# Kernel optimization log

Hardware: AMD Instinct MI355X
Metric: run time of the kernel (lower is better)

## Reference

```python
import jax, jax.numpy as jnp
import numpy as np

B, S, D, H = 4, 1024, 1024, 16
HD = D // H


def setup_inputs() -> dict:
    key = jax.random.key(0)
    ks = jax.random.split(key, 12)
    s = 1.0 / np.sqrt(D)
    inp = {
        'q': jax.random.normal(ks[0], (B, S, D), jnp.float32),
        'k': jax.random.normal(ks[1], (B, S, D), jnp.float32),
        'v': jax.random.normal(ks[2], (B, S, D), jnp.float32),
        'mask': jnp.broadcast_to(jnp.tril(jnp.ones((S, S), jnp.int32)), (B, S, S)),
        'Wq': jax.random.uniform(ks[3], (D, D), jnp.float32, -s, s),
        'bq': jax.random.uniform(ks[4], (D,), jnp.float32, -s, s),
        'Wk': jax.random.uniform(ks[5], (D, D), jnp.float32, -s, s),
        'bk': jax.random.uniform(ks[6], (D,), jnp.float32, -s, s),
        'Wv': jax.random.uniform(ks[7], (D, D), jnp.float32, -s, s),
        'bv': jax.random.uniform(ks[8], (D,), jnp.float32, -s, s),
        'Wo': jax.random.uniform(ks[9], (D, D), jnp.float32, -s, s),
        'bo': jax.random.uniform(ks[10], (D,), jnp.float32, -s, s),
    }
    return inp


def _split_heads(x):
    # [B,S,D] -> [B,H,S,HD]
    b, s, d = x.shape
    return x.reshape(b, s, H, HD).transpose(0, 2, 1, 3)


def reference(q, k, v, mask, Wq, bq, Wk, bk, Wv, bv, Wo, bo):
    # Linear projections (torch Linear: x @ W.T + b) followed by relu
    qh = jax.nn.relu(q @ Wq.T + bq)
    kh = jax.nn.relu(k @ Wk.T + bk)
    vh = jax.nn.relu(v @ Wv.T + bv)
    qh, kh, vh = _split_heads(qh), _split_heads(kh), _split_heads(vh)
    scores = jnp.einsum('bhqd,bhkd->bhqk', qh, kh) / jnp.sqrt(jnp.float32(HD))
    scores = jnp.where(mask[:, None, :, :] == 0, jnp.float32(-1e9), scores)
    attn = jax.nn.softmax(scores, axis=-1)
    y = jnp.einsum('bhqk,bhkd->bhqd', attn, vh)
    y = y.transpose(0, 2, 1, 3).reshape(B, S, D)  # merge heads
    return jax.nn.relu(y @ Wo.T + bo)
```

## Files before the change

kernel.cpp:

```cpp
#include <hip/hip_runtime.h>


using f16    = _Float16;
using f16x4  = __attribute__((ext_vector_type(4))) _Float16;
using f16x8  = __attribute__((ext_vector_type(8))) _Float16;
using f32x4  = __attribute__((ext_vector_type(4))) float;
using f32x16 = __attribute__((ext_vector_type(16))) float;

static constexpr int S = 1024, Dm = 1024, NH = 16, HD = 64;

#if __has_builtin(__builtin_amdgcn_mfma_f32_32x32x8f16)
#define USE_MFMA32 1
#define MFMA32(ACC, A_, B_) \
    (ACC) = __builtin_amdgcn_mfma_f32_32x32x8f16((A_), (B_), (ACC), 0, 0, 0)
#else
#define USE_MFMA32 0
#endif
#if __has_builtin(__builtin_amdgcn_mfma_f32_16x16x16f16)
#define USE_MFMA 1
#define MFMA16(ACC, A_, B_) \
    (ACC) = __builtin_amdgcn_mfma_f32_16x16x16f16((A_), (B_), (ACC), 0, 0, 0)
#else
#define USE_MFMA 0
#endif

#define LO4(v) __builtin_shufflevector((v), (v), 0, 1, 2, 3)
#define HI4(v) __builtin_shufflevector((v), (v), 4, 5, 6, 7)

__device__ __forceinline__ f16x4 cvt4(float4 a) {
    f16x4 r; r[0] = (f16)a.x; r[1] = (f16)a.y; r[2] = (f16)a.z; r[3] = (f16)a.w;
    return r;
}
__device__ __forceinline__ int pcol64(int k) {
    return ((k >> 2) & 3) * 16 + ((k >> 4) << 2) + (k & 3);
}

__device__ __forceinline__ void store_out(void* out, int mode, int m, int n, float v) {
    if (mode == 2) {
        ((float*)out)[(size_t)m * Dm + n] = v;
    } else {
        const int b_ = m >> 10, s_ = m & 1023, h_ = n >> 6, hd_ = n & 63;
        const size_t idx = (mode == 0)
            ? (((size_t)(b_ * NH + h_) * S + s_) * HD + pcol64(hd_))
            : (((size_t)(b_ * NH + h_) * HD + hd_) * S + s_);
        ((f16*)out)[idx] = (f16)v;
    }
}

template <int AF32>
__device__ __forceinline__ void gemm_core(const void* __restrict__ A,
                                          const float* __restrict__ W,
                                          const float* __restrict__ bias,
                                          void* __restrict__ out, int mode)
{
    const int tid = threadIdx.x;
    const int bm = blockIdx.x, bn = blockIdx.y;
#if USE_MFMA32
    __shared__ alignas(16) f16 As[2][128][36];
    __shared__ alignas(16) f16 Ws[2][128][36];

    const int lane = tid & 63, wave = tid >> 6;
    const int l31 = lane & 31, kh = lane >> 5;
    const int wm = wave & 1, wn = wave >> 1;

    const int ar = tid >> 3, ac = (tid & 7) * 4;
    const int ar2 = tid >> 2, ac2 = (tid & 3) * 8;
    const float* Af = (const float*)A + (size_t)(bm * 128 + ar) * Dm + ac;
    const f16*   Ah = (const f16*)A   + (size_t)(bm * 128 + ar2) * Dm + ac2;
    const float* Wf = W + (size_t)(bn * 128 + ar) * Dm + ac;

    float4 pa[4]; uint4 pah[2]; float4 pw[4];
    auto pref = [&](int k0) {
        if (AF32) {
#pragma unroll
            for (int i = 0; i < 4; ++i) pa[i] = *(const float4*)(Af + k0 + (size_t)i * 32 * Dm);
        } else {
#pragma unroll
            for (int i = 0; i < 2; ++i) pah[i] = *(const uint4*)(Ah + k0 + (size_t)i * 64 * Dm);
        }
#pragma unroll
        for (int i = 0; i < 4; ++i) pw[i] = *(const float4*)(Wf + k0 + (size_t)i * 32 * Dm);
    };
    auto stage = [&](int cur) {
        if (AF32) {
#pragma unroll
            for (int i = 0; i < 4; ++i) *(f16x4*)&As[cur][ar + i * 32][ac] = cvt4(pa[i]);
        } else {
#pragma unroll
            for (int i = 0; i < 2; ++i) *(f16x8*)&As[cur][ar2 + i * 64][ac2] = *(f16x8*)&pah[i];
        }
#pragma unroll
        for (int i = 0; i < 4; ++i) *(f16x4*)&Ws[cur][ar + i * 32][ac] = cvt4(pw[i]);
    };

    f32x16 acc[2][2] = {};
    pref(0);
    for (int it = 0; it < Dm / 32; ++it) {
        const int cur = it & 1;
        stage(cur);
        __syncthreads();
        if (it < Dm / 32 - 1) pref((it + 1) * 32);

#pragma unroll
        for (int s = 0; s < 4; ++s) {
            f16x4 af[2], bf[2];
            const int c = s * 8 + kh * 4;
            af[0] = *(const f16x4*)&As[cur][wm * 64 + l31][c];
            af[1] = *(const f16x4*)&As[cur][wm * 64 + 32 + l31][c];
            bf[0] = *(const f16x4*)&Ws[cur][wn * 64 + l31][c];
            bf[1] = *(const f16x4*)&Ws[cur][wn * 64 + 32 + l31][c];
            MFMA32(acc[0][0], af[0], bf[0]);
            MFMA32(acc[0][1], af[0], bf[1]);
            MFMA32(acc[1][0], af[1], bf[0]);
            MFMA32(acc[1][1], af[1], bf[1]);
        }
    }

#pragma unroll
    for (int g2 = 0; g2 < 2; ++g2) {
        const int col = bn * 128 + wn * 64 + g2 * 32 + l31;
        const float bb = bias[col];
#pragma unroll
        for (int g = 0; g < 2; ++g)
#pragma unroll
            for (int blk = 0; blk < 4; ++blk) {
                const int row0 = bm * 128 + wm * 64 + g * 32 + 8 * blk + 4 * kh;
                if (mode == 1) {
                    const int b_ = row0 >> 10, s_ = row0 & 1023;
                    const int h_ = col >> 6, hd_ = col & 63;
                    f16x4 v;
#pragma unroll
                    for (int r = 0; r < 4; ++r)
                        v[r] = (f16)fmaxf(acc[g][g2][blk * 4 + r] + bb, 0.0f);
                    *(f16x4*)&((f16*)out)[((size_t)(b_ * NH + h_) * HD + hd_) * S + s_] = v;
                } else {
#pragma unroll
                    for (int r = 0; r < 4; ++r)
                        store_out(out, mode, row0 + r, col,
                                  fmaxf(acc[g][g2][blk * 4 + r] + bb, 0.0f));
                }
            }
    }
#else
    for (int i = tid; i < 128 * 128; i += 256) {
        const int m = bm * 128 + (i >> 7);
        const int n = bn * 128 + (i & 127);
        float acc = 0.0f;
        for (int k = 0; k < Dm; ++k) {
            const float a = AF32 ? ((const float*)A)[(size_t)m * Dm + k]
                                 : (float)((const f16*)A)[(size_t)m * Dm + k];
            acc = fmaf(a, W[(size_t)n * Dm + k], acc);
        }
        store_out(out, mode, m, n, fmaxf(acc + bias[n], 0.0f));
    }
#endif
}

__global__ __launch_bounds__(256)
void gemm_qkv(const float* __restrict__ q, const float* __restrict__ k,
              const float* __restrict__ v,
              const float* __restrict__ Wq, const float* __restrict__ Wk,
              const float* __restrict__ Wv,
              const float* __restrict__ bq, const float* __restrict__ bk,
              const float* __restrict__ bv,
              f16* __restrict__ qh, f16* __restrict__ kh, f16* __restrict__ vt)
{
    const int z = blockIdx.z;
    const float* A = (z == 0) ? q : (z == 1) ? k : v;
    const float* W = (z == 0) ? Wq : (z == 1) ? Wk : Wv;
    const float* B = (z == 0) ? bq : (z == 1) ? bk : bv;
    f16* O = (z == 0) ? qh : (z == 1) ? kh : vt;
    gemm_core<1>(A, W, B, O, (z == 2) ? 1 : 0);
}

__global__ __launch_bounds__(256)
void gemm_out(const f16* __restrict__ y, const float* __restrict__ Wo,
              const float* __restrict__ bo, float* __restrict__ out)
{
    gemm_core<0>(y, Wo, bo, out, 2);
}

__global__ __launch_bounds__(256)
void attn_fwd(const f16* __restrict__ qh, const f16* __restrict__ kh,
              const f16* __restrict__ vt, f16* __restrict__ y)
{
    const int bz = blockIdx.x;
    const int qt = bz & 15;
    const int h  = (bz >> 4) & 15;
    const int b  = bz >> 8;
    const size_t head = (size_t)(b * NH + h) * S * HD;

#if USE_MFMA
    __shared__ alignas(16) f16 Ks[2][64][72];
    __shared__ alignas(16) f16 Vs[2][64][72];

    const int tid  = threadIdx.x;
    const int wave = tid >> 6;
    const int lane = tid & 63;
    const int l15  = lane & 15;
    const int quad = lane >> 4;
    const int sr   = tid >> 2;
    const int sc   = (tid & 3) * 16;

    const f16* Qrow = qh + head + (size_t)(qt * 64 + wave * 16 + l15) * HD;
    const f16* Kp   = kh + head;
    const f16* Vp   = vt + head;

    f16x4 aq[4];
    {
        const uint4 q0 = *(const uint4*)(Qrow + quad * 16);
        const uint4 q1 = *(const uint4*)(Qrow + quad * 16 + 8);
        aq[0] = *(f16x4*)((f16*)&q0);
        aq[1] = *(f16x4*)((f16*)&q0 + 4);
        aq[2] = *(f16x4*)((f16*)&q1);
        aq[3] = *(f16x4*)((f16*)&q1 + 4);
    }

    const int qg = qt * 64 + wave * 16 + l15;
    float m_i = -1e30f, l_i = 0.0f;
    f32x4 acc_o[4] = {};

    uint4 pk[2], pv[2];
    auto pref = [&](int kt) {
        const f16* Kr = Kp + (size_t)(kt * 64 + sr) * HD + sc;
        pk[0] = *(const uint4*)Kr;
        pk[1] = *(const uint4*)(Kr + 8);
        const f16* Vr = Vp + (size_t)sr * S + kt * 64 + sc;
        pv[0] = *(const uint4*)Vr;
        pv[1] = *(const uint4*)(Vr + 8);
    };

    pref(0);
    for (int kt = 0; kt <= qt; ++kt) {
        const int cur = kt & 1;
        *(uint4*)&Ks[cur][sr][sc]     = pk[0];
        *(uint4*)&Ks[cur][sr][sc + 8] = pk[1];
        {
            const int sb = (sc >> 4) * 4;
            *(f16x4*)&Vs[cur][sr][0 * 16 + sb] = *(f16x4*)((f16*)&pv[0]);
            *(f16x4*)&Vs[cur][sr][1 * 16 + sb] = *(f16x4*)((f16*)&pv[0] + 4);
            *(f16x4*)&Vs[cur][sr][2 * 16 + sb] = *(f16x4*)((f16*)&pv[1]);
            *(f16x4*)&Vs[cur][sr][3 * 16 + sb] = *(f16x4*)((f16*)&pv[1] + 4);
        }
        __syncthreads();
        if (kt < qt) pref(kt + 1);

        f32x4 accs[4] = {};
#pragma unroll
        for (int t = 0; t < 4; ++t) {
            const f16x8 k8a = *(const f16x8*)&Ks[cur][t * 16 + l15][quad * 16];
            const f16x8 k8b = *(const f16x8*)&Ks[cur][t * 16 + l15][quad * 16 + 8];
            MFMA16(accs[t], LO4(k8a), aq[0]);
            MFMA16(accs[t], HI4(k8a), aq[1]);
            MFMA16(accs[t], LO4(k8b), aq[2]);
            MFMA16(accs[t], HI4(k8b), aq[3]);
        }

        const int key0 = kt * 64 + quad * 4;
#pragma unroll
        for (int t = 0; t < 4; ++t)
#pragma unroll
            for (int r = 0; r < 4; ++r) {
                float sv = accs[t][r] * 0.125f;
                if (key0 + t * 16 + r > qg) sv = -1e9f;
                accs[t][r] = sv;
            }

        float mx = accs[0][0];
#pragma unroll
        for (int t = 0; t < 4; ++t)
#pragma unroll
            for (int r = 0; r < 4; ++r) mx = fmaxf(mx, accs[t][r]);
        mx = fmaxf(mx, __shfl_xor(mx, 16, 64));
        mx = fmaxf(mx, __shfl_xor(mx, 32, 64));
        const float mnew = fmaxf(m_i, mx);
        float sm = 0.0f;
#pragma unroll
        for (int t = 0; t < 4; ++t)
#pragma unroll
            for (int r = 0; r < 4; ++r) {
                const float e = __expf(accs[t][r] - mnew);
                accs[t][r] = e;
                sm += e;
            }
        sm += __shfl_xor(sm, 16, 64);
        sm += __shfl_xor(sm, 32, 64);
        const float alpha = __expf(m_i - mnew);
        l_i = l_i * alpha + sm;
        m_i = mnew;

        f16x4 ap[4];
#pragma unroll
        for (int c = 0; c < 4; ++c) {
            f16x4 v;
#pragma unroll
            for (int j = 0; j < 4; ++j) v[j] = (f16)accs[c][j];
            ap[c] = v;
        }

        float ar[4];
#pragma unroll
        for (int r = 0; r < 4; ++r) ar[r] = __shfl(alpha, quad * 4 + r, 64);
#pragma unroll
        for (int t2 = 0; t2 < 4; ++t2)
#pragma unroll
            for (int r = 0; r < 4; ++r) acc_o[t2][r] *= ar[r];
#pragma unroll
        for (int t2 = 0; t2 < 4; ++t2) {
            const f16x8 v8a = *(const f16x8*)&Vs[cur][t2 * 16 + l15][quad * 16];
            const f16x8 v8b = *(const f16x8*)&Vs[cur][t2 * 16 + l15][quad * 16 + 8];
            MFMA16(acc_o[t2], ap[0], LO4(v8a));
            MFMA16(acc_o[t2], ap[1], HI4(v8a));
            MFMA16(acc_o[t2], ap[2], LO4(v8b));
            MFMA16(acc_o[t2], ap[3], HI4(v8b));
        }
    }

    float lr[4];
#pragma unroll
    for (int r = 0; r < 4; ++r) lr[r] = __shfl(l_i, quad * 4 + r, 64);
#pragma unroll
    for (int t2 = 0; t2 < 4; ++t2)
#pragma unroll
        for (int r = 0; r < 4; ++r) {
            const int srow = qt * 64 + wave * 16 + quad * 4 + r;
            const int dcol = h * 64 + t2 * 16 + l15;
            y[((size_t)b * S + srow) * Dm + dcol] = (f16)(acc_o[t2][r] / lr[r]);
        }
#else
    const int tid = threadIdx.x;
    if (tid < 64) {
        const int q = qt * 64 + tid;
        const f16* Qr = qh + head + (size_t)q * HD;
        float qv[64];
        for (int d = 0; d < 64; ++d) qv[d] = (float)Qr[d];
        float mx = -1e30f;
        for (int key = 0; key <= q; ++key) {
            const f16* Kr = kh + head + (size_t)key * HD;
            float s = 0.0f;
            for (int d = 0; d < 64; ++d) s = fmaf(qv[d], (float)Kr[d], s);
            mx = fmaxf(mx, s * 0.125f);
        }
        float o[64];
        for (int d = 0; d < 64; ++d) o[d] = 0.0f;
        float l = 0.0f;
        for (int key = 0; key <= q; ++key) {
            const f16* Kr = kh + head + (size_t)key * HD;
            float s = 0.0f;
            for (int d = 0; d < 64; ++d) s = fmaf(qv[d], (float)Kr[d], s);
            const float p = __expf(s * 0.125f - mx);
            l += p;
            for (int d = 0; d < 64; ++d)
                o[d] = fmaf(p, (float)vt[head + (size_t)d * S + key], o[d]);
        }
        for (int d = 0; d < 64; ++d)
            y[((size_t)b * S + q) * Dm + h * 64 + d] = (f16)(o[d] / l);
    }
#endif
}

extern "C" void kernel_launch(void* const* d_in, const int* in_sizes, int n_in,
                              void* d_out, int out_size, void* d_ws, size_t ws_size,
                              hipStream_t stream)
{
    f16* ws = (f16*)d_ws;
    const size_t SEG = (size_t)4 * 1024 * 1024;
    f16* qh = ws;
    f16* kh = ws + SEG;
    f16* vt = ws + 2 * SEG;
    f16* y  = ws + 3 * SEG;

    gemm_qkv<<<dim3(32, 8, 3), 256, 0, stream>>>(
        (const float*)d_in[0], (const float*)d_in[1], (const float*)d_in[2],
        (const float*)d_in[4], (const float*)d_in[6], (const float*)d_in[8],
        (const float*)d_in[5], (const float*)d_in[7], (const float*)d_in[9],
        qh, kh, vt);
    attn_fwd<<<dim3(4 * NH * (S / 64)), 256, 0, stream>>>(qh, kh, vt, y);
    gemm_out<<<dim3(32, 8), 256, 0, stream>>>(
        y, (const float*)d_in[10], (const float*)d_in[11], (float*)d_out);
}
```

Baseline: 277.2 us.

## Permute GEMM shared-memory K layout for 128-bit fragment reads and deepen A prefetch

Stores A and W tiles into shared memory with a permuted K-column order and a padded row stride, so each lane can fetch its MFMA fragments with two 16-byte LDS reads instead of four 8-byte reads. A operand global loads are prefetched two iterations ahead using a double register buffer, while W stays one iteration ahead. The goal is fewer LDS instructions and better hiding of global latency, paid for with extra registers and possible new bank conflicts on the split stores. This relies on the LO4/HI4 helpers and on the permutation matching the MFMA k ordering.

```diff
diff --git a/kernel.cpp b/kernel.cpp
--- a/kernel.cpp
+++ b/kernel.cpp
@@ -56,63 +56,80 @@
     const int tid = threadIdx.x;
     const int bm = blockIdx.x, bn = blockIdx.y;
 #if USE_MFMA32
-    __shared__ alignas(16) f16 As[2][128][36];
-    __shared__ alignas(16) f16 Ws[2][128][36];
+    __shared__ alignas(16) f16 As[2][128][40];
+    __shared__ alignas(16) f16 Ws[2][128][40];
 
     const int lane = tid & 63, wave = tid >> 6;
-    const int l31 = lane & 31, kh = lane >> 5;
+    const int l31 = lane & 31, khalf = lane >> 5;
     const int wm = wave & 1, wn = wave >> 1;
 
     const int ar = tid >> 3, ac = (tid & 7) * 4;
+    const int pA = (((ac >> 2) & 1) << 4) + ((ac >> 3) << 2);
     const int ar2 = tid >> 2, ac2 = (tid & 3) * 8;
+    const int pH = (ac2 >> 3) << 2;
+
     const float* Af = (const float*)A + (size_t)(bm * 128 + ar) * Dm + ac;
     const f16*   Ah = (const f16*)A   + (size_t)(bm * 128 + ar2) * Dm + ac2;
     const float* Wf = W + (size_t)(bn * 128 + ar) * Dm + ac;
 
-    float4 pa[4]; uint4 pah[2]; float4 pw[4];
-    auto pref = [&](int k0) {
+    float4 pa[2][4]; uint4 pah[2][2]; float4 pw[4];
+    auto prefA = [&](int d, int k0) {
         if (AF32) {
 #pragma unroll
-            for (int i = 0; i < 4; ++i) pa[i] = *(const float4*)(Af + k0 + (size_t)i * 32 * Dm);
+            for (int i = 0; i < 4; ++i) pa[d][i] = *(const float4*)(Af + k0 + (size_t)i * 32 * Dm);
         } else {
 #pragma unroll
-            for (int i = 0; i < 2; ++i) pah[i] = *(const uint4*)(Ah + k0 + (size_t)i * 64 * Dm);
-        }
+            for (int i = 0; i < 2; ++i) pah[d][i] = *(const uint4*)(Ah + k0 + (size_t)i * 64 * Dm);
+        }
+    };
+    auto prefW = [&](int k0) {
 #pragma unroll
         for (int i = 0; i < 4; ++i) pw[i] = *(const float4*)(Wf + k0 + (size_t)i * 32 * Dm);
     };
-    auto stage = [&](int cur) {
+    auto stage = [&](int cur, int d) {
         if (AF32) {
 #pragma unroll
-            for (int i = 0; i < 4; ++i) *(f16x4*)&As[cur][ar + i * 32][ac] = cvt4(pa[i]);
+            for (int i = 0; i < 4; ++i) *(f16x4*)&As[cur][ar + i * 32][pA] = cvt4(pa[d][i]);
         } else {
 #pragma unroll
-            for (int i = 0; i < 2; ++i) *(f16x8*)&As[cur][ar2 + i * 64][ac2] = *(f16x8*)&pah[i];
-        }
-#pragma unroll
-        for (int i = 0; i < 4; ++i) *(f16x4*)&Ws[cur][ar + i * 32][ac] = cvt4(pw[i]);
+            for (int i = 0; i < 2; ++i) {
+                const f16* src = (const f16*)&pah[d][i];
+                *(f16x4*)&As[cur][ar2 + i * 64][pH]      = *(const f16x4*)src;
+                *(f16x4*)&As[cur][ar2 + i * 64][16 + pH] = *(const f16x4*)(src + 4);
+            }
+        }
+#pragma unroll
+        for (int i = 0; i < 4; ++i) *(f16x4*)&Ws[cur][ar + i * 32][pA] = cvt4(pw[i]);
     };
 
     f32x16 acc[2][2] = {};
-    pref(0);
+    prefA(0, 0); prefW(0);
+    prefA(1, 32);
     for (int it = 0; it < Dm / 32; ++it) {
         const int cur = it & 1;
-        stage(cur);
+        stage(cur, cur);
         __syncthreads();
-        if (it < Dm / 32 - 1) pref((it + 1) * 32);
-
-#pragma unroll
-        for (int s = 0; s < 4; ++s) {
-            f16x4 af[2], bf[2];
-            const int c = s * 8 + kh * 4;
-            af[0] = *(const f16x4*)&As[cur][wm * 64 + l31][c];
-            af[1] = *(const f16x4*)&As[cur][wm * 64 + 32 + l31][c];
-            bf[0] = *(const f16x4*)&Ws[cur][wn * 64 + l31][c];
-            bf[1] = *(const f16x4*)&Ws[cur][wn * 64 + 32 + l31][c];
-            MFMA32(acc[0][0], af[0], bf[0]);
-            MFMA32(acc[0][1], af[0], bf[1]);
-            MFMA32(acc[1][0], af[1], bf[0]);
-            MFMA32(acc[1][1], af[1], bf[1]);
+        if (it + 2 < Dm / 32) prefA(cur, (it + 2) * 32);
+        if (it + 1 < Dm / 32) prefW((it + 1) * 32);
+
+        f16x8 a8[2][2], w8[2][2];
+#pragma unroll
+        for (int g = 0; g < 2; ++g) {
+            a8[g][0] = *(const f16x8*)&As[cur][wm * 64 + g * 32 + l31][khalf * 16];
+            a8[g][1] = *(const f16x8*)&As[cur][wm * 64 + g * 32 + l31][khalf * 16 + 8];
+            w8[g][0] = *(const f16x8*)&Ws[cur][wn * 64 + g * 32 + l31][khalf * 16];
+            w8[g][1] = *(const f16x8*)&Ws[cur][wn * 64 + g * 32 + l31][khalf * 16 + 8];
+        }
+#pragma unroll
+        for (int hf = 0; hf < 2; ++hf) {
+            MFMA32(acc[0][0], LO4(a8[0][hf]), LO4(w8[0][hf]));
+            MFMA32(acc[0][1], LO4(a8[0][hf]), LO4(w8[1][hf]));
+            MFMA32(acc[1][0], LO4(a8[1][hf]), LO4(w8[0][hf]));
+            MFMA32(acc[1][1], LO4(a8[1][hf]), LO4(w8[1][hf]));
+            MFMA32(acc[0][0], HI4(a8[0][hf]), HI4(w8[0][hf]));
+            MFMA32(acc[0][1], HI4(a8[0][hf]), HI4(w8[1][hf]));
+            MFMA32(acc[1][0], HI4(a8[1][hf]), HI4(w8[0][hf]));
+            MFMA32(acc[1][1], HI4(a8[1][hf]), HI4(w8[1][hf]));
         }
     }
 
@@ -124,7 +141,7 @@
         for (int g = 0; g < 2; ++g)
 #pragma unroll
             for (int blk = 0; blk < 4; ++blk) {
-                const int row0 = bm * 128 + wm * 64 + g * 32 + 8 * blk + 4 * kh;
+                const int row0 = bm * 128 + wm * 64 + g * 32 + 8 * blk + 4 * khalf;
                 if (mode == 1) {
                     const int b_ = row0 >> 10, s_ = row0 & 1023;
                     const int h_ = col >> 6, hd_ = col & 63;
```

Result: slower. 407.4 us (+46.9%).
